# Optimization experiments

Hardware: AMD Instinct MI355X
Metric: run time of the kernel (lower is better)

Reference implementation:

```python
import math
import jax, jax.numpy as jnp
import numpy as np

V, BS, L, C, H, B, T = 50257, 2048, 4, 768, 12, 2, 2048
D = C // H


def layer_norm(x, g, b, eps=1e-5):
    m = x.mean(-1, keepdims=True)
    v = ((x - m) ** 2).mean(-1, keepdims=True)
    return (x - m) / jnp.sqrt(v + eps) * g + b


def setup_inputs() -> dict:
    key = jax.random.key(0)
    ks = jax.random.split(key, 10)
    s = 0.02
    inp = {}
    inp["idx"] = jax.random.randint(ks[0], (B, T), 0, V)
    inp["tok_emb"] = jax.random.normal(ks[1], (V, C), jnp.float32) * s
    inp["pos_emb"] = jax.random.normal(ks[2], (BS, C), jnp.float32) * s
    inp["ln1_g"] = jnp.ones((L, C)); inp["ln1_b"] = jnp.zeros((L, C))
    inp["qkv_w"] = jax.random.normal(ks[3], (L, C, 3 * C), jnp.float32) * s
    inp["qkv_b"] = jnp.zeros((L, 3 * C))
    inp["aproj_w"] = jax.random.normal(ks[4], (L, C, C), jnp.float32) * s
    inp["aproj_b"] = jnp.zeros((L, C))
    inp["ln2_g"] = jnp.ones((L, C)); inp["ln2_b"] = jnp.zeros((L, C))
    inp["fc_w"] = jax.random.normal(ks[5], (L, C, 4 * C), jnp.float32) * s
    inp["fc_b"] = jnp.zeros((L, 4 * C))
    inp["mproj_w"] = jax.random.normal(ks[6], (L, 4 * C, C), jnp.float32) * s
    inp["mproj_b"] = jnp.zeros((L, C))
    inp["lnf_g"] = jnp.ones((C,)); inp["lnf_b"] = jnp.zeros((C,))
    inp["head_w"] = jax.random.normal(ks[7], (C, V), jnp.float32) * s
    return inp


def reference(idx, tok_emb, pos_emb, ln1_g, ln1_b, qkv_w, qkv_b, aproj_w, aproj_b,
              ln2_g, ln2_b, fc_w, fc_b, mproj_w, mproj_b, lnf_g, lnf_b, head_w):
    b, t = idx.shape
    x = tok_emb[idx] + pos_emb[:t][None]  # [B,T,C]; dropout p=0 -> identity
    mask = jnp.tril(jnp.ones((t, t), bool))  # causal
    neg_inf = jnp.finfo(x.dtype).min
    n_layer = qkv_w.shape[0]
    for l in range(n_layer):
        h = layer_norm(x, ln1_g[l], ln1_b[l])
        qkv = h @ qkv_w[l] + qkv_b[l]  # [B,T,3C]
        q, k, v = jnp.split(qkv, 3, axis=-1)
        q = q.reshape(b, t, H, D).transpose(0, 2, 1, 3)  # [B,H,T,D]
        k = k.reshape(b, t, H, D).transpose(0, 2, 1, 3)
        v = v.reshape(b, t, H, D).transpose(0, 2, 1, 3)
        att = jnp.einsum('bhqd,bhkd->bhqk', q, k) / math.sqrt(D)
        att = jnp.where(mask, att, neg_inf)
        att = jax.nn.softmax(att, axis=-1)
        y = jnp.einsum('bhqk,bhkd->bhqd', att, v)
        y = y.transpose(0, 2, 1, 3).reshape(b, t, C)
        x = x + (y @ aproj_w[l] + aproj_b[l])
        h2 = layer_norm(x, ln2_g[l], ln2_b[l])
        hid = jax.nn.gelu(h2 @ fc_w[l] + fc_b[l], approximate=False)  # exact erf GELU (torch default)
        x = x + (hid @ mproj_w[l] + mproj_b[l])
    x = layer_norm(x, lnf_g, lnf_b)
    logits = x @ head_w  # [B,T,V]
    return logits
```

## Files before the change

### kernel.cpp

```cpp
#include <hip/hip_runtime.h>
#include <cstdint>
#include <cstddef>

#define Tn 2048
#define Bn 2
#define Hn 12
#define Cn 768
#define Ln 4
#define Vn 50257

typedef unsigned short ushort_t;
typedef __attribute__((ext_vector_type(8))) __bf16 bf16x8;
typedef __attribute__((ext_vector_type(8))) unsigned short u16x8;
typedef __attribute__((ext_vector_type(4))) float f32x4;

static constexpr size_t QKV_ELEMS = (size_t)Bn * Hn * Tn * 64;

__device__ inline unsigned short f2bf(float f) {
  unsigned int u = __float_as_uint(f);
  unsigned int r = (u + 0x7fffu + ((u >> 16) & 1u)) >> 16;
  return (unsigned short)r;
}

__device__ inline f32x4 zero4() { f32x4 z; z[0]=0.f; z[1]=0.f; z[2]=0.f; z[3]=0.f; return z; }

__device__ inline void gload_lds16(const ushort_t* g, ushort_t* l) {
  __builtin_amdgcn_global_load_lds(
      (const __attribute__((address_space(1))) void*)g,
      (__attribute__((address_space(3))) void*)l, 16, 0, 0);
}

__device__ inline int swz_lin() {
  int nbm = gridDim.x;
  int lin = blockIdx.y * nbm + blockIdx.x;
  int nwg = nbm * gridDim.y;
  int q = nwg >> 3, r = nwg & 7, x = lin & 7, p = lin >> 3;
  return (x < r ? x * (q + 1) : r * (q + 1) + (x - r) * q) + p;
}

__global__ __launch_bounds__(256) void embed_kernel(const int* __restrict__ idx,
    const float* __restrict__ tok, const float* __restrict__ pos, float* __restrict__ x) {
  int row = blockIdx.x;
  int t = row & (Tn - 1);
  int token = idx[row];
  const float* tr = tok + (size_t)token * Cn;
  const float* pr = pos + (size_t)t * Cn;
  float* xr = x + (size_t)row * Cn;
  for (int c = threadIdx.x; c < Cn; c += 256) xr[c] = tr[c] + pr[c];
}

__global__ __launch_bounds__(256) void ln_kernel(const float* __restrict__ x,
    const float* __restrict__ gam, const float* __restrict__ bet, ushort_t* __restrict__ out) {
  int row = blockIdx.x;
  const float* xr = x + (size_t)row * Cn;
  float v[3]; float s = 0.f, s2 = 0.f;
  #pragma unroll
  for (int e = 0; e < 3; ++e) { float t = xr[threadIdx.x + e*256]; v[e] = t; s += t; s2 += t*t; }
  #pragma unroll
  for (int off = 32; off >= 1; off >>= 1) { s += __shfl_xor(s, off); s2 += __shfl_xor(s2, off); }
  __shared__ float red[8];
  int w = threadIdx.x >> 6;
  if ((threadIdx.x & 63) == 0) { red[w] = s; red[4 + w] = s2; }
  __syncthreads();
  s  = red[0] + red[1] + red[2] + red[3];
  s2 = red[4] + red[5] + red[6] + red[7];
  float mean = s * (1.f / Cn);
  float var  = s2 * (1.f / Cn) - mean * mean;
  float rstd = rsqrtf(var + 1e-5f);
  ushort_t* orow = out + (size_t)row * Cn;
  #pragma unroll
  for (int e = 0; e < 3; ++e) {
    int c = threadIdx.x + e*256;
    orow[c] = f2bf((v[e] - mean) * rstd * gam[c] + bet[c]);
  }
}

__global__ __launch_bounds__(256) void tcvt_kernel(const float* __restrict__ in,
    ushort_t* __restrict__ out, int K, int N, int Npad) {
  __shared__ float tile[32][33];
  int n0 = blockIdx.x * 32, k0 = blockIdx.y * 32;
  int tx = threadIdx.x, ty = threadIdx.y;
  #pragma unroll
  for (int r = 0; r < 4; ++r) {
    int k = k0 + ty + 8*r;
    int n = n0 + tx;
    tile[ty + 8*r][tx] = (n < N) ? in[(size_t)k * N + n] : 0.f;
  }
  __syncthreads();
  #pragma unroll
  for (int r = 0; r < 4; ++r) {
    int n = n0 + ty + 8*r;
    out[(size_t)n * K + k0 + tx] = f2bf(tile[tx][ty + 8*r]);
  }
}

__global__ __launch_bounds__(256) void vtrans_kernel(const ushort_t* __restrict__ vin,
                                                     ushort_t* __restrict__ vout) {
  __shared__ ushort_t tile[64][65];
  int t0 = blockIdx.x * 64;
  size_t bh = blockIdx.y;
  const ushort_t* src = vin + (bh * Tn + t0) * 64;
  int row = threadIdx.x >> 2, c0 = (threadIdx.x & 3) * 16;
  u16x8 a = *(const u16x8*)&src[(size_t)row * 64 + c0];
  u16x8 b = *(const u16x8*)&src[(size_t)row * 64 + c0 + 8];
  #pragma unroll
  for (int j = 0; j < 8; ++j) { tile[row][c0 + j] = a[j]; tile[row][c0 + 8 + j] = b[j]; }
  __syncthreads();
  int d = threadIdx.x >> 2, tq = (threadIdx.x & 3) * 16;
  u16x8 o0, o1;
  #pragma unroll
  for (int j = 0; j < 8; ++j) { o0[j] = tile[tq + j][d]; o1[j] = tile[tq + 8 + j][d]; }
  ushort_t* dst = vout + (bh * 64 + d) * Tn + t0 + tq;
  *(u16x8*)&dst[0] = o0;
  *(u16x8*)&dst[8] = o1;
}

template<int MODE, int TM>
__global__ __launch_bounds__(256) void gemm_kernel(
    const ushort_t* __restrict__ A, const ushort_t* __restrict__ Bt,
    const float* __restrict__ bias, void* __restrict__ outp,
    const float* __restrict__ res, int M, int N, int K) {
  constexpr int MI = TM / 32;
  __shared__ ushort_t As[TM * 32];
  __shared__ ushort_t Bs[128 * 32];
  const int t = threadIdx.x;
  int nl = swz_lin();
  const int bm = nl % gridDim.x;
  const int bn = nl / gridDim.x;
  const int w = t >> 6, l = t & 63, lo = l & 15, g = l >> 4;
  const int wm = w >> 1, wn = w & 1;

  f32x4 acc[MI][4];
  #pragma unroll
  for (int i = 0; i < MI; ++i)
    #pragma unroll
    for (int j = 0; j < 4; ++j) acc[i][j] = zero4();

  const int srow = t >> 2;
  const int scol = (t & 3) * 8;
  const ushort_t* gA = A  + (size_t)(bm * TM  + srow) * K + scol;
  const ushort_t* gB = Bt + (size_t)(bn * 128 + srow) * K + scol;
  ushort_t* lA = As + w * 512;
  ushort_t* lB = Bs + w * 512;

  for (int k0 = 0; k0 < K; k0 += 32) {
    __syncthreads();
    gload_lds16(gA + k0, lA);
    if (TM == 128) gload_lds16(gA + (size_t)64 * K + k0, lA + 2048);
    gload_lds16(gB + k0, lB);
    gload_lds16(gB + (size_t)64 * K + k0, lB + 2048);
    __syncthreads();
    bf16x8 af[MI], bfr[4];
    #pragma unroll
    for (int mi = 0; mi < MI; ++mi)
      af[mi] = *(const bf16x8*)&As[(size_t)(wm*(TM/2) + mi*16 + lo) * 32 + g*8];
    #pragma unroll
    for (int ni = 0; ni < 4; ++ni)
      bfr[ni] = *(const bf16x8*)&Bs[(size_t)(wn*64 + ni*16 + lo) * 32 + g*8];
    #pragma unroll
    for (int mi = 0; mi < MI; ++mi)
      #pragma unroll
      for (int ni = 0; ni < 4; ++ni)
        acc[mi][ni] = __builtin_amdgcn_mfma_f32_16x16x32_bf16(af[mi], bfr[ni], acc[mi][ni], 0, 0, 0);
  }

  #pragma unroll
  for (int mi = 0; mi < MI; ++mi) {
    #pragma unroll
    for (int ni = 0; ni < 4; ++ni) {
      int colg = bn*128 + wn*64 + ni*16 + lo;
      if (colg < N) {
        float bv = bias ? bias[colg] : 0.f;
        #pragma unroll
        for (int i = 0; i < 4; ++i) {
          int rowg = bm*TM + wm*(TM/2) + mi*16 + 4*g + i;
          float vv = acc[mi][ni][i] + bv;
          if (MODE == 0) {
            ((float*)outp)[(size_t)rowg * N + colg] = vv;
          } else if (MODE == 1) {
            size_t off = (size_t)rowg * N + colg;
            ((float*)outp)[off] = res[off] + vv;
          } else if (MODE == 2) {
            float ge = 0.5f * vv * (1.f + erff(vv * 0.70710678118f));
            ((ushort_t*)outp)[(size_t)rowg * N + colg] = f2bf(ge);
          } else {
            int which = colg / Cn;
            int rem = colg - which * Cn;
            int h = rem >> 6, d = rem & 63;
            int b = rowg >> 11, tt = rowg & (Tn - 1);
            ushort_t* qb = (ushort_t*)outp;
            size_t bh = (size_t)(b * Hn + h);
            size_t off = (bh * Tn + tt) * 64 + d;
            if (which == 0)      qb[off] = f2bf(vv * 0.125f);
            else if (which == 1) qb[QKV_ELEMS + off] = f2bf(vv);
            else                 qb[3*QKV_ELEMS + off] = f2bf(vv);
          }
        }
      }
    }
  }
}

__global__ __launch_bounds__(64) void attn_kernel(const ushort_t* __restrict__ qkvh,
                                                  ushort_t* __restrict__ y) {
  const int l = threadIdx.x;
  const int lo = l & 15, g = l >> 4;
  int nl = swz_lin();
  const int qt = nl & 127;
  const int bh = nl >> 7;
  const int b = bh / Hn, h = bh % Hn;
  const int q0 = qt * 16;
  const ushort_t* Qp = qkvh + (size_t)bh * Tn * 64;
  const ushort_t* Kp = qkvh + QKV_ELEMS + (size_t)bh * Tn * 64;
  const ushort_t* Vt = qkvh + 2*QKV_ELEMS + (size_t)bh * 64 * Tn;

  bf16x8 qf[2];
  #pragma unroll
  for (int ch = 0; ch < 2; ++ch)
    qf[ch] = *(const bf16x8*)&Qp[(size_t)(q0 + lo) * 64 + ch*32 + g*8];

  f32x4 of[4];
  #pragma unroll
  for (int ch = 0; ch < 4; ++ch) of[ch] = zero4();
  float m = -1e30f, lsum = 0.f;
  const int nkv = q0 + 16;
  const bool ghi = (g >= 2);
  const int lg2 = (g & 1) * 32;

  for (int kv0 = 0; kv0 < nkv; kv0 += 32) {
    bf16x8 vf[4];
    #pragma unroll
    for (int ch = 0; ch < 4; ++ch)
      vf[ch] = *(const bf16x8*)&Vt[(size_t)(ch*16 + lo) * Tn + kv0 + g*8];

    float s8[8];
    #pragma unroll
    for (int sub = 0; sub < 2; ++sub) {
      int kvb = kv0 + 16*sub;
      bf16x8 kf[2];
      #pragma unroll
      for (int ch = 0; ch < 2; ++ch)
        kf[ch] = *(const bf16x8*)&Kp[(size_t)(kvb + lo) * 64 + ch*32 + g*8];
      f32x4 st = zero4();
      st = __builtin_amdgcn_mfma_f32_16x16x32_bf16(kf[0], qf[0], st, 0, 0, 0);
      st = __builtin_amdgcn_mfma_f32_16x16x32_bf16(kf[1], qf[1], st, 0, 0, 0);
      #pragma unroll
      for (int i = 0; i < 4; ++i) {
        int kvi = kvb + 4*g + i;
        s8[sub*4 + i] = (kvi <= q0 + lo) ? st[i] : -1e30f;
      }
    }
    float tmax = s8[0];
    #pragma unroll
    for (int j = 1; j < 8; ++j) tmax = fmaxf(tmax, s8[j]);
    tmax = fmaxf(tmax, __shfl_xor(tmax, 16));
    tmax = fmaxf(tmax, __shfl_xor(tmax, 32));
    float newm = fmaxf(m, tmax);
    float resc = __expf(m - newm);
    float p8[8]; float psum = 0.f;
    #pragma unroll
    for (int j = 0; j < 8; ++j) { p8[j] = __expf(s8[j] - newm); psum += p8[j]; }
    psum += __shfl_xor(psum, 16);
    psum += __shfl_xor(psum, 32);
    lsum = lsum * resc + psum;
    m = newm;
    #pragma unroll
    for (int i = 0; i < 4; ++i) {
      float rs = __shfl(resc, 4*g + i);
      of[0][i] *= rs; of[1][i] *= rs; of[2][i] *= rs; of[3][i] *= rs;
    }
    unsigned int q4[4];
    #pragma unroll
    for (int c = 0; c < 4; ++c)
      q4[c] = (unsigned int)f2bf(p8[2*c]) | ((unsigned int)f2bf(p8[2*c+1]) << 16);
    union { unsigned int wv[4]; bf16x8 v; } pu;
    #pragma unroll
    for (int j = 0; j < 4; ++j) {
      int srcLane = lo + lg2 + ((j >> 1) << 4);
      unsigned int lo_w = (unsigned int)__shfl((int)q4[j & 1], srcLane);
      unsigned int hi_w = (unsigned int)__shfl((int)q4[2 + (j & 1)], srcLane);
      pu.wv[j] = ghi ? hi_w : lo_w;
    }
    #pragma unroll
    for (int ch = 0; ch < 4; ++ch)
      of[ch] = __builtin_amdgcn_mfma_f32_16x16x32_bf16(pu.v, vf[ch], of[ch], 0, 0, 0);
  }

  #pragma unroll
  for (int i = 0; i < 4; ++i) {
    float li = 1.f / __shfl(lsum, 4*g + i);
    of[0][i] *= li; of[1][i] *= li; of[2][i] *= li; of[3][i] *= li;
  }
  ushort_t* yb = y + ((size_t)b*Tn + q0) * Cn + h*64;
  #pragma unroll
  for (int ch = 0; ch < 4; ++ch)
    #pragma unroll
    for (int i = 0; i < 4; ++i)
      yb[(size_t)(4*g + i) * Cn + ch*16 + lo] = f2bf(of[ch][i]);
}

extern "C" void kernel_launch(void* const* d_in, const int* in_sizes, int n_in,
                              void* d_out, int out_size, void* d_ws, size_t ws_size,
                              hipStream_t stream) {
  const int*   idx     = (const int*)d_in[0];
  const float* tok_emb = (const float*)d_in[1];
  const float* pos_emb = (const float*)d_in[2];
  const float* ln1_g   = (const float*)d_in[3];
  const float* ln1_b   = (const float*)d_in[4];
  const float* qkv_w   = (const float*)d_in[5];
  const float* qkv_b   = (const float*)d_in[6];
  const float* aproj_w = (const float*)d_in[7];
  const float* aproj_b = (const float*)d_in[8];
  const float* ln2_g   = (const float*)d_in[9];
  const float* ln2_b   = (const float*)d_in[10];
  const float* fc_w    = (const float*)d_in[11];
  const float* fc_b    = (const float*)d_in[12];
  const float* mproj_w = (const float*)d_in[13];
  const float* mproj_b = (const float*)d_in[14];
  const float* lnf_g   = (const float*)d_in[15];
  const float* lnf_b   = (const float*)d_in[16];
  const float* head_w  = (const float*)d_in[17];
  float* out = (float*)d_out;

  char* ws = (char*)d_ws;
  float*    x    = (float*)(ws);
  ushort_t* hA   = (ushort_t*)(ws + 12582912);
  ushort_t* hB   = (ushort_t*)(ws + 18874368);
  ushort_t* qkvh = (ushort_t*)(ws + 44040192);
  ushort_t* wT   = (ushort_t*)(ws + 69206016);

  const int M = Bn * Tn;
  dim3 tb(32, 8);

  embed_kernel<<<M, 256, 0, stream>>>(idx, tok_emb, pos_emb, x);
  for (int l = 0; l < Ln; ++l) {
    ln_kernel<<<M, 256, 0, stream>>>(x, ln1_g + l*Cn, ln1_b + l*Cn, hA);
    tcvt_kernel<<<dim3(2304/32, 768/32), tb, 0, stream>>>(qkv_w + (size_t)l*Cn*3*Cn, wT, 768, 2304, 2304);
    gemm_kernel<3,128><<<dim3(M/128, 2304/128), 256, 0, stream>>>(hA, wT, qkv_b + (size_t)l*3*Cn, qkvh, nullptr, M, 2304, 768);
    vtrans_kernel<<<dim3(Tn/64, Bn*Hn), 256, 0, stream>>>(qkvh + 3*QKV_ELEMS, qkvh + 2*QKV_ELEMS);
    attn_kernel<<<dim3(128, Bn*Hn), 64, 0, stream>>>(qkvh, hA);
    tcvt_kernel<<<dim3(768/32, 768/32), tb, 0, stream>>>(aproj_w + (size_t)l*Cn*Cn, wT, 768, 768, 768);
    gemm_kernel<1,64><<<dim3(M/64, 768/128), 256, 0, stream>>>(hA, wT, aproj_b + (size_t)l*Cn, x, x, M, 768, 768);
    ln_kernel<<<M, 256, 0, stream>>>(x, ln2_g + l*Cn, ln2_b + l*Cn, hA);
    tcvt_kernel<<<dim3(3072/32, 768/32), tb, 0, stream>>>(fc_w + (size_t)l*Cn*4*Cn, wT, 768, 3072, 3072);
    gemm_kernel<2,128><<<dim3(M/128, 3072/128), 256, 0, stream>>>(hA, wT, fc_b + (size_t)l*4*Cn, hB, nullptr, M, 3072, 768);
    tcvt_kernel<<<dim3(768/32, 3072/32), tb, 0, stream>>>(mproj_w + (size_t)l*4*Cn*Cn, wT, 3072, 768, 768);
    gemm_kernel<1,64><<<dim3(M/64, 768/128), 256, 0, stream>>>(hB, wT, mproj_b + (size_t)l*Cn, x, x, M, 768, 3072);
  }
  ln_kernel<<<M, 256, 0, stream>>>(x, lnf_g, lnf_b, hA);
  tcvt_kernel<<<dim3(50304/32, 768/32), tb, 0, stream>>>(head_w, wT, 768, Vn, 50304);
  gemm_kernel<0,128><<<dim3(M/128, 50304/128), 256, 0, stream>>>(hA, wT, nullptr, out, nullptr, M, Vn, 768);
}
```

Before: 1.919 ms.

## Double-buffer GEMM LDS tiles and group block rasterization for L2 reuse

```diff
diff --git a/kernel.cpp b/kernel.cpp
--- a/kernel.cpp
+++ b/kernel.cpp
@@ -121,12 +121,22 @@
     const float* __restrict__ bias, void* __restrict__ outp,
     const float* __restrict__ res, int M, int N, int K) {
   constexpr int MI = TM / 32;
-  __shared__ ushort_t As[TM * 32];
-  __shared__ ushort_t Bs[128 * 32];
+  constexpr int ABUF = TM * 32;
+  __shared__ ushort_t As[2 * ABUF];
+  __shared__ ushort_t Bs[2 * 4096];
   const int t = threadIdx.x;
-  int nl = swz_lin();
-  const int bm = nl % gridDim.x;
-  const int bn = nl / gridDim.x;
+
+  int bm, bn;
+  {
+    int seq = swz_lin();
+    const int G = 8;
+    int NBN = gridDim.y;
+    int gsz = G * NBN;
+    int grp = seq / gsz;
+    int t2 = seq - grp * gsz;
+    bn = t2 / G;
+    bm = grp * G + (t2 - bn * G);
+  }
   const int w = t >> 6, l = t & 63, lo = l & 15, g = l >> 4;
   const int wm = w >> 1, wn = w & 1;
 
@@ -143,26 +153,38 @@
   ushort_t* lA = As + w * 512;
   ushort_t* lB = Bs + w * 512;
 
-  for (int k0 = 0; k0 < K; k0 += 32) {
-    __syncthreads();
-    gload_lds16(gA + k0, lA);
-    if (TM == 128) gload_lds16(gA + (size_t)64 * K + k0, lA + 2048);
-    gload_lds16(gB + k0, lB);
-    gload_lds16(gB + (size_t)64 * K + k0, lB + 2048);
-    __syncthreads();
+  auto stage = [&](int buf, int k0) {
+    gload_lds16(gA + k0, lA + buf * ABUF);
+    if (TM == 128) gload_lds16(gA + (size_t)64 * K + k0, lA + buf * ABUF + 2048);
+    gload_lds16(gB + k0, lB + buf * 4096);
+    gload_lds16(gB + (size_t)64 * K + k0, lB + buf * 4096 + 2048);
+  };
+  auto compute = [&](int buf) {
+    const ushort_t* as = As + buf * ABUF;
+    const ushort_t* bs = Bs + buf * 4096;
     bf16x8 af[MI], bfr[4];
     #pragma unroll
     for (int mi = 0; mi < MI; ++mi)
-      af[mi] = *(const bf16x8*)&As[(size_t)(wm*(TM/2) + mi*16 + lo) * 32 + g*8];
+      af[mi] = *(const bf16x8*)&as[(size_t)(wm*(TM/2) + mi*16 + lo) * 32 + g*8];
     #pragma unroll
     for (int ni = 0; ni < 4; ++ni)
-      bfr[ni] = *(const bf16x8*)&Bs[(size_t)(wn*64 + ni*16 + lo) * 32 + g*8];
+      bfr[ni] = *(const bf16x8*)&bs[(size_t)(wn*64 + ni*16 + lo) * 32 + g*8];
     #pragma unroll
     for (int mi = 0; mi < MI; ++mi)
       #pragma unroll
       for (int ni = 0; ni < 4; ++ni)
         acc[mi][ni] = __builtin_amdgcn_mfma_f32_16x16x32_bf16(af[mi], bfr[ni], acc[mi][ni], 0, 0, 0);
-  }
+  };
+
+  const int NK = K >> 5;
+  stage(0, 0);
+  __syncthreads();
+  for (int kk = 0; kk < NK - 1; ++kk) {
+    stage((kk + 1) & 1, (kk + 1) << 5);
+    compute(kk & 1);
+    __syncthreads();
+  }
+  compute((NK - 1) & 1);
 
   #pragma unroll
   for (int mi = 0; mi < MI; ++mi) {
```

Measured after the change: 1.852 ms. 1.04x faster.
